# Kernel tuning notes

Measured on AMD Instinct MI355X. Metric: run time of the kernel, lower is better.

The kernel has to match this reference:

```python
import jax, jax.numpy as jnp
import numpy as np

N, E = 20000, 320000
IN, H, C = 1024, 8, 64
HC = H * C
EDGE_DIM = 16
NUM_GRAPHS = 8
LEAKY_SLOPE = 0.2
LN_EPS = 1e-5


def setup_inputs() -> dict:
    key = jax.random.key(0)
    ks = jax.random.split(key, 12)
    s = 0.05
    return {
        "x": jax.random.normal(ks[0], (N, IN), jnp.float32),
        "edge_attr": jax.random.normal(ks[1], (E, EDGE_DIM), jnp.float32),
        "edge_index": jax.random.randint(ks[2], (2, E), 0, N, dtype=jnp.int64),
        "batch": jnp.sort(jax.random.randint(ks[3], (N,), 0, NUM_GRAPHS, dtype=jnp.int64)),
        "W_src": jax.random.normal(ks[4], (IN, HC), jnp.float32) * s,
        "W_dst": jax.random.normal(ks[5], (IN, HC), jnp.float32) * s,
        "att_src": jax.random.normal(ks[6], (H, C), jnp.float32) * s,
        "att_dst": jax.random.normal(ks[7], (H, C), jnp.float32) * s,
        "bias": jnp.zeros((HC,), jnp.float32),
        "ln_gamma": jnp.ones((HC,), jnp.float32),
        "ln_beta": jnp.zeros((HC,), jnp.float32),
        "prelu_a": jnp.full((HC,), 0.25, jnp.float32),
    }


def reference(x, edge_attr, edge_index, batch, W_src, W_dst, att_src, att_dst,
              bias, ln_gamma, ln_beta, prelu_a):
    # Eval mode: node/edge feature dropout and attention dropout are identity.
    # with_edge == 'N': edge_attr is unused by the conv.
    n = x.shape[0]
    src, dst = edge_index[0], edge_index[1]

    xs = (x @ W_src).reshape(n, H, C)   # source-side projections
    xd = (x @ W_dst).reshape(n, H, C)   # dest-side projections
    a_src = jnp.einsum('nhc,hc->nh', xs, att_src)
    a_dst = jnp.einsum('nhc,hc->nh', xd, att_dst)

    # edge scores + softmax over incoming edges of each destination node
    e = jax.nn.leaky_relu(a_src[src] + a_dst[dst], LEAKY_SLOPE)  # [E,H]
    m = jax.ops.segment_max(e, dst, num_segments=n)              # [N,H]
    m = jax.lax.stop_gradient(jnp.where(jnp.isfinite(m), m, 0.0))
    ex = jnp.exp(e - m[dst])
    denom = jax.ops.segment_sum(ex, dst, num_segments=n)
    alpha = ex / (denom[dst] + 1e-16)                            # [E,H]

    msg = alpha[:, :, None] * xs[src]                            # [E,H,C]
    out = jax.ops.segment_sum(msg, dst, num_segments=n).reshape(n, HC) + bias

    # norm_type == 'layer': the per-graph boolean-mask loop applies LayerNorm
    # row-wise; with sorted batch ids this equals a single LayerNorm over all
    # nodes (LayerNorm has no cross-row statistics).
    mu = jnp.mean(out, axis=-1, keepdims=True)
    var = jnp.mean(jnp.square(out - mu), axis=-1, keepdims=True)
    y = (out - mu) * jax.lax.rsqrt(var + LN_EPS) * ln_gamma + ln_beta

    # PReLU with per-channel slope
    return jnp.where(y >= 0, y, prelu_a * y)
```

## Files before the change

kernel.cpp:

```cpp
#include <hip/hip_runtime.h>
#include <hip/hip_bf16.h>

#define N_NODES 20000
#define N_EDGES 320000
#define IN_DIM  1024
#define H_HEADS 8
#define C_CH    64
#define HC      512
#define LEAKY   0.2f
#define LN_EPS  1e-5f

#define BCOLS 576

typedef short bf16x8 __attribute__((ext_vector_type(8)));
typedef float f32x4  __attribute__((ext_vector_type(4)));

__device__ __forceinline__ unsigned short f2bf(float f) {
    union { float f; unsigned int u; } c; c.f = f;
    unsigned int u = c.u;
    unsigned int r = (u + 0x7fffu + ((u >> 16) & 1u)) >> 16;
    return (unsigned short)r;
}
__device__ __forceinline__ float bf2f(unsigned int h) {
    union { unsigned int u; float f; } c; c.u = h << 16; return c.f;
}
__device__ __forceinline__ void gload_lds16(const void* g, void* l) {
    __builtin_amdgcn_global_load_lds(
        (const __attribute__((address_space(1))) unsigned int*)g,
        (__attribute__((address_space(3))) unsigned int*)l, 16, 0, 0);
}

#define DEG_BLOCKS 1250

__global__ __launch_bounds__(256) void deg_hist(
        const int* __restrict__ ei, int* __restrict__ deg) {
    int e = blockIdx.x * 256 + threadIdx.x;
    atomicAdd(&deg[ei[N_EDGES + e]], 1);
}

#define CONV_BLOCKS 2048
#define PREP_BLOCKS 1024

__global__ __launch_bounds__(256) void mid_pass(
        const float* __restrict__ x, short* __restrict__ xb,
        const float* __restrict__ Wsrc, const float* __restrict__ Wdst,
        const float* __restrict__ att_src, const float* __restrict__ att_dst,
        short* __restrict__ wbT,
        const int* __restrict__ deg, int* __restrict__ off,
        int* __restrict__ cursor) {
    int t   = threadIdx.x;
    int bid = blockIdx.x;

    if (bid < CONV_BLOCKS) {
        const int total = N_NODES * IN_DIM / 8;
        int stride = CONV_BLOCKS * 256;
        for (int i = bid * 256 + t; i < total; i += stride) {
            float4 a = ((const float4*)x)[(size_t)i * 2];
            float4 b = ((const float4*)x)[(size_t)i * 2 + 1];
            uint4 r;
            r.x = (unsigned int)f2bf(a.x) | ((unsigned int)f2bf(a.y) << 16);
            r.y = (unsigned int)f2bf(a.z) | ((unsigned int)f2bf(a.w) << 16);
            r.z = (unsigned int)f2bf(b.x) | ((unsigned int)f2bf(b.y) << 16);
            r.w = (unsigned int)f2bf(b.z) | ((unsigned int)f2bf(b.w) << 16);
            *(uint4*)(&xb[(size_t)i * 8]) = r;
        }
        return;
    }

    if (bid < CONV_BLOCKS + PREP_BLOCKS) {
        if (t >= 128) return;
        int k = bid - CONV_BLOCKS;
        float4 v = *(const float4*)(Wsrc + (size_t)k * HC + t * 4);
        wbT[(size_t)(t * 4 + 0) * IN_DIM + k] = (short)f2bf(v.x);
        wbT[(size_t)(t * 4 + 1) * IN_DIM + k] = (short)f2bf(v.y);
        wbT[(size_t)(t * 4 + 2) * IN_DIM + k] = (short)f2bf(v.z);
        wbT[(size_t)(t * 4 + 3) * IN_DIM + k] = (short)f2bf(v.w);
        if (t < 16) {
            int h = t & 7;
            const float* W   = (t < 8) ? Wsrc : Wdst;
            const float* att = (t < 8) ? att_src : att_dst;
            float s = 0.f;
            #pragma unroll
            for (int c = 0; c < C_CH; ++c)
                s += W[(size_t)k * HC + h * C_CH + c] * att[h * C_CH + c];
            wbT[(size_t)(512 + t) * IN_DIM + k] = (short)f2bf(s);
        } else if (t < 64) {
            wbT[(size_t)(512 + t) * IN_DIM + k] = 0;
        }
        return;
    }

    if (t >= 128) return;
    __shared__ int wtot[2];
    int lane = t & 63, w = t >> 6;
    const int4* deg4 = (const int4*)deg;
    int s = 0;
    if (t < 125) {
        #pragma unroll
        for (int j = 0; j < 40; ++j) {
            int4 u = deg4[t * 40 + j];
            s += u.x + u.y + u.z + u.w;
        }
    }
    int v = s;
    #pragma unroll
    for (int o = 1; o < 64; o <<= 1) {
        int u = __shfl_up(v, o);
        if (lane >= o) v += u;
    }
    if (lane == 63) wtot[w] = v;
    __syncthreads();
    int add = (w == 1) ? wtot[0] : 0;
    int run = add + v - s;
    if (t < 125) {
        int4* off4 = (int4*)off;
        int4* cur4 = (int4*)cursor;
        #pragma unroll
        for (int j = 0; j < 40; ++j) {
            int4 u = deg4[t * 40 + j];
            int4 o_;
            o_.x = run;
            o_.y = o_.x + u.x;
            o_.z = o_.y + u.y;
            o_.w = o_.z + u.z;
            off4[t * 40 + j] = o_;
            cur4[t * 40 + j] = o_;
            run = o_.w + u.w;
        }
        if (t == 124) off[N_NODES] = run;
    }
}

#define BM 64
#define BN 96
#define BK 64
#define NCOLT (BCOLS / BN)
#define NROWT ((N_NODES + BM - 1) / BM)
#define NWG (NCOLT * NROWT)
#define KSTEPS (IN_DIM / BK)
#define A_SLOTS (BM * BK / 8)
#define B_SLOTS (BN * BK / 8)

__global__ __launch_bounds__(256) void gemm_scatter(
        const short* __restrict__ xb,
        const short* __restrict__ wbT,
        short* __restrict__ xsb,
        float* __restrict__ a_srcv,
        float* __restrict__ a_dstv,
        const int* __restrict__ ei,
        int* __restrict__ cursor,
        int* __restrict__ csr_src) {
    __shared__ short As[A_SLOTS * 8];
    __shared__ short Bs[B_SLOTS * 8];

    int t = threadIdx.x;

    if (blockIdx.x >= NWG) {
        int e = (blockIdx.x - NWG) * 256 + t;
        int d = ei[N_EDGES + e];
        int idx = atomicAdd(&cursor[d], 1);
        csr_src[idx] = ei[e];
        return;
    }

    int orig = blockIdx.x;
    const int q = NWG >> 3, r = NWG & 7;
    int xcd  = orig & 7;
    int wgid = (xcd < r ? xcd * (q + 1) : r * (q + 1) + (xcd - r) * q) + (orig >> 3);
    int col0 = (wgid % NCOLT) * BN;
    int row0 = (wgid / NCOLT) * BM;

    int lane = t & 63;
    int w    = t >> 6;
    int lr   = lane & 15;
    int lg   = lane >> 4;
    int sw   = lr & 7;
    int wr   = (w >> 1) * 32;
    int wc   = (w & 1) * 48;

    const short* a_base[2];
    #pragma unroll
    for (int i = 0; i < 2; ++i) {
        int s  = t + 256 * i;
        int m  = s >> 3;
        int kc = (s & 7) ^ (m & 7);
        int gm = row0 + m;
        if (gm >= N_NODES) gm = N_NODES - 1;
        a_base[i] = xb + (size_t)gm * IN_DIM + kc * 8;
    }
    const short* b_base[3];
    #pragma unroll
    for (int i = 0; i < 3; ++i) {
        int s  = t + 256 * i;
        int c  = s >> 3;
        int kc = (s & 7) ^ (c & 7);
        b_base[i] = wbT + (size_t)(col0 + c) * IN_DIM + kc * 8;
    }

    f32x4 acc[2][3] = {};

    for (int step = 0; step < KSTEPS; ++step) {
        int k0 = step * BK;
        #pragma unroll
        for (int i = 0; i < 2; ++i)
            gload_lds16(a_base[i] + k0, &As[(t + 256 * i) * 8]);
        #pragma unroll
        for (int i = 0; i < 3; ++i)
            gload_lds16(b_base[i] + k0, &Bs[(t + 256 * i) * 8]);
        asm volatile("s_waitcnt vmcnt(0)" ::: "memory");
        __builtin_amdgcn_s_barrier();

        #pragma unroll
        for (int ks = 0; ks < 2; ++ks) {
            int kc  = ks * 4 + lg;
            int kca = kc ^ sw;
            bf16x8 af[2], bfr[3];
            #pragma unroll
            for (int mi = 0; mi < 2; ++mi)
                af[mi] = *(const bf16x8*)(&As[((wr + mi * 16 + lr) * 8 + kca) * 8]);
            #pragma unroll
            for (int ni = 0; ni < 3; ++ni)
                bfr[ni] = *(const bf16x8*)(&Bs[((wc + ni * 16 + lr) * 8 + kca) * 8]);
            __builtin_amdgcn_s_setprio(1);
            #pragma unroll
            for (int mi = 0; mi < 2; ++mi)
                #pragma unroll
                for (int ni = 0; ni < 3; ++ni)
                    acc[mi][ni] = __builtin_amdgcn_mfma_f32_16x16x32_bf16(
                        af[mi], bfr[ni], acc[mi][ni], 0, 0, 0);
            __builtin_amdgcn_s_setprio(0);
        }
        __builtin_amdgcn_s_barrier();
    }

    #pragma unroll
    for (int mi = 0; mi < 2; ++mi) {
        #pragma unroll
        for (int rr = 0; rr < 4; ++rr) {
            int row = row0 + wr + mi * 16 + lg * 4 + rr;
            if (row >= N_NODES) continue;
            #pragma unroll
            for (int ni = 0; ni < 3; ++ni) {
                int col = col0 + wc + ni * 16 + lr;
                float v = acc[mi][ni][rr];
                if (col < 512)      xsb[(size_t)row * HC + col] = (short)f2bf(v);
                else if (col < 520) a_srcv[(size_t)row * 8 + (col - 512)] = v;
                else if (col < 528) a_dstv[(size_t)row * 8 + (col - 520)] = v;
            }
        }
    }
}

__global__ __launch_bounds__(256) void aggregate_ln(
        const int* __restrict__ off,
        const int* __restrict__ csr_src,
        const float* __restrict__ a_srcv,
        const float* __restrict__ a_dstv,
        const short* __restrict__ xsb,
        const float* __restrict__ bias,
        const float* __restrict__ gamma,
        const float* __restrict__ beta,
        const float* __restrict__ prelu_a,
        float* __restrict__ out) {
    int lane = threadIdx.x & 63;
    int n    = blockIdx.x * 4 + (threadIdx.x >> 6);
    int ch0  = lane * 8;
    int h    = lane >> 3;

    int start = off[n], end = off[n + 1];
    float ad  = a_dstv[(size_t)n * 8 + h];

    float acc[8] = {};
    float wsum = 0.f;

#define EDGE_ACC(sv)                                                          \
    do {                                                                      \
        float sc_ = a_srcv[(size_t)(sv) * 8 + h] + ad;                        \
        uint4 u_  = *(const uint4*)(xsb + (size_t)(sv) * HC + ch0);           \
        sc_ = (sc_ >= 0.f) ? sc_ : LEAKY * sc_;                               \
        float w_ = __expf(sc_);                                               \
        acc[0] = fmaf(w_, bf2f(u_.x & 0xffffu), acc[0]);                      \
        acc[1] = fmaf(w_, bf2f(u_.x >> 16),     acc[1]);                      \
        acc[2] = fmaf(w_, bf2f(u_.y & 0xffffu), acc[2]);                      \
        acc[3] = fmaf(w_, bf2f(u_.y >> 16),     acc[3]);                      \
        acc[4] = fmaf(w_, bf2f(u_.z & 0xffffu), acc[4]);                      \
        acc[5] = fmaf(w_, bf2f(u_.z >> 16),     acc[5]);                      \
        acc[6] = fmaf(w_, bf2f(u_.w & 0xffffu), acc[6]);                      \
        acc[7] = fmaf(w_, bf2f(u_.w >> 16),     acc[7]);                      \
        wsum += w_;                                                           \
    } while (0)

    int i = start;
    for (; i + 3 < end; i += 4) {
        int s0 = __builtin_amdgcn_readfirstlane(csr_src[i]);
        int s1 = __builtin_amdgcn_readfirstlane(csr_src[i + 1]);
        int s2 = __builtin_amdgcn_readfirstlane(csr_src[i + 2]);
        int s3 = __builtin_amdgcn_readfirstlane(csr_src[i + 3]);
        EDGE_ACC(s0); EDGE_ACC(s1); EDGE_ACC(s2); EDGE_ACC(s3);
    }
    for (; i < end; ++i) {
        int s0 = __builtin_amdgcn_readfirstlane(csr_src[i]);
        EDGE_ACC(s0);
    }
#undef EDGE_ACC

    float inv = 1.f / (wsum + 1e-16f);
    float4 b0 = *(const float4*)(bias + ch0);
    float4 b1 = *(const float4*)(bias + ch0 + 4);
    float v8[8];
    float psum = 0.f, psq = 0.f;
    const float bb[8] = {b0.x, b0.y, b0.z, b0.w, b1.x, b1.y, b1.z, b1.w};
    #pragma unroll
    for (int j = 0; j < 8; ++j) {
        v8[j] = acc[j] * inv + bb[j];
        psum += v8[j];
        psq  += v8[j] * v8[j];
    }
    #pragma unroll
    for (int o = 32; o > 0; o >>= 1) {
        psum += __shfl_xor(psum, o);
        psq  += __shfl_xor(psq, o);
    }
    float mu   = psum * (1.f / (float)HC);
    float var  = psq * (1.f / (float)HC) - mu * mu;
    float rstd = rsqrtf(var + LN_EPS);

    float4 g0 = *(const float4*)(gamma + ch0);
    float4 g1 = *(const float4*)(gamma + ch0 + 4);
    float4 e0 = *(const float4*)(beta + ch0);
    float4 e1 = *(const float4*)(beta + ch0 + 4);
    float4 p0 = *(const float4*)(prelu_a + ch0);
    float4 p1 = *(const float4*)(prelu_a + ch0 + 4);
    const float gg[8] = {g0.x, g0.y, g0.z, g0.w, g1.x, g1.y, g1.z, g1.w};
    const float ee[8] = {e0.x, e0.y, e0.z, e0.w, e1.x, e1.y, e1.z, e1.w};
    const float pp[8] = {p0.x, p0.y, p0.z, p0.w, p1.x, p1.y, p1.z, p1.w};
    float y[8];
    #pragma unroll
    for (int j = 0; j < 8; ++j) {
        float v = (v8[j] - mu) * rstd * gg[j] + ee[j];
        y[j] = (v >= 0.f) ? v : pp[j] * v;
    }
    float4* o4 = (float4*)(out + (size_t)n * HC + ch0);
    o4[0] = make_float4(y[0], y[1], y[2], y[3]);
    o4[1] = make_float4(y[4], y[5], y[6], y[7]);
}

extern "C" void kernel_launch(void* const* d_in, const int* in_sizes, int n_in,
                              void* d_out, int out_size, void* d_ws, size_t ws_size,
                              hipStream_t stream) {
    const float* x        = (const float*)d_in[0];
    const int*   ei       = (const int*)d_in[2];
    const float* Wsrc     = (const float*)d_in[4];
    const float* Wdst     = (const float*)d_in[5];
    const float* att_src  = (const float*)d_in[6];
    const float* att_dst  = (const float*)d_in[7];
    const float* bias     = (const float*)d_in[8];
    const float* gamma    = (const float*)d_in[9];
    const float* beta     = (const float*)d_in[10];
    const float* prelu_a  = (const float*)d_in[11];
    float* out            = (float*)d_out;

    char*  ws = (char*)d_ws;
    size_t o  = 0;
    auto alloc = [&](size_t bytes) -> void* {
        void* p = ws + o;
        o += (bytes + 255) & ~(size_t)255;
        return p;
    };
    short* wbT     = (short*)alloc(sizeof(short) * BCOLS * IN_DIM);
    short* xsb     = (short*)alloc(sizeof(short) * (size_t)N_NODES * HC);
    float* a_srcv  = (float*)alloc(sizeof(float) * N_NODES * 8);
    float* a_dstv  = (float*)alloc(sizeof(float) * N_NODES * 8);
    int*   deg     = (int*)alloc(sizeof(int) * N_NODES);
    int*   off     = (int*)alloc(sizeof(int) * (N_NODES + 1));
    int*   cursor  = (int*)alloc(sizeof(int) * N_NODES);
    int*   csr_src = (int*)alloc(sizeof(int) * N_EDGES);

    short* xb = (short*)d_out;

    hipMemsetAsync(deg, 0, sizeof(int) * N_NODES, stream);

    deg_hist<<<DEG_BLOCKS, 256, 0, stream>>>(ei, deg);

    mid_pass<<<CONV_BLOCKS + PREP_BLOCKS + 1, 256, 0, stream>>>(
        x, xb, Wsrc, Wdst, att_src, att_dst, wbT, deg, off, cursor);

    gemm_scatter<<<NWG + DEG_BLOCKS, 256, 0, stream>>>(
        xb, wbT, xsb, a_srcv, a_dstv, ei, cursor, csr_src);

    aggregate_ln<<<N_NODES / 4, 256, 0, stream>>>(
        off, csr_src, a_srcv, a_dstv, xsb, bias, gamma, beta, prelu_a, out);
}
```

Before: 152.9 us.

## Fuse fp32-to-bf16 conversion of x into GEMM A-tile load, widen N tile

```diff
diff --git a/kernel.cpp b/kernel.cpp
--- a/kernel.cpp
+++ b/kernel.cpp
@@ -24,6 +24,11 @@
 __device__ __forceinline__ float bf2f(unsigned int h) {
     union { unsigned int u; float f; } c; c.u = h << 16; return c.f;
 }
+__device__ __forceinline__ unsigned int cvtpk(float lo, float hi) {
+    unsigned int r;
+    asm("v_cvt_pk_bf16_f32 %0, %1, %2" : "=v"(r) : "v"(lo), "v"(hi));
+    return r;
+}
 __device__ __forceinline__ void gload_lds16(const void* g, void* l) {
     __builtin_amdgcn_global_load_lds(
         (const __attribute__((address_space(1))) unsigned int*)g,
@@ -38,101 +43,80 @@
     atomicAdd(&deg[ei[N_EDGES + e]], 1);
 }
 
-#define CONV_BLOCKS 2048
-#define PREP_BLOCKS 1024
-
-__global__ __launch_bounds__(256) void mid_pass(
-        const float* __restrict__ x, short* __restrict__ xb,
-        const float* __restrict__ Wsrc, const float* __restrict__ Wdst,
-        const float* __restrict__ att_src, const float* __restrict__ att_dst,
-        short* __restrict__ wbT,
-        const int* __restrict__ deg, int* __restrict__ off,
-        int* __restrict__ cursor) {
-    int t   = threadIdx.x;
-    int bid = blockIdx.x;
-
-    if (bid < CONV_BLOCKS) {
-        const int total = N_NODES * IN_DIM / 8;
-        int stride = CONV_BLOCKS * 256;
-        for (int i = bid * 256 + t; i < total; i += stride) {
-            float4 a = ((const float4*)x)[(size_t)i * 2];
-            float4 b = ((const float4*)x)[(size_t)i * 2 + 1];
-            uint4 r;
-            r.x = (unsigned int)f2bf(a.x) | ((unsigned int)f2bf(a.y) << 16);
-            r.y = (unsigned int)f2bf(a.z) | ((unsigned int)f2bf(a.w) << 16);
-            r.z = (unsigned int)f2bf(b.x) | ((unsigned int)f2bf(b.y) << 16);
-            r.w = (unsigned int)f2bf(b.z) | ((unsigned int)f2bf(b.w) << 16);
-            *(uint4*)(&xb[(size_t)i * 8]) = r;
+__global__ void prep_w_scan(const float* __restrict__ Wsrc,
+                            const float* __restrict__ Wdst,
+                            const float* __restrict__ att_src,
+                            const float* __restrict__ att_dst,
+                            short* __restrict__ wbT,
+                            const int* __restrict__ deg,
+                            int* __restrict__ off,
+                            int* __restrict__ cursor) {
+    int t = threadIdx.x;
+
+    if (blockIdx.x == IN_DIM) {
+        __shared__ int wtot[2];
+        int lane = t & 63, w = t >> 6;
+        const int4* deg4 = (const int4*)deg;
+        int s = 0;
+        if (t < 125) {
+            #pragma unroll
+            for (int j = 0; j < 40; ++j) {
+                int4 u = deg4[t * 40 + j];
+                s += u.x + u.y + u.z + u.w;
+            }
+        }
+        int v = s;
+        #pragma unroll
+        for (int o = 1; o < 64; o <<= 1) {
+            int u = __shfl_up(v, o);
+            if (lane >= o) v += u;
+        }
+        if (lane == 63) wtot[w] = v;
+        __syncthreads();
+        int add = (w == 1) ? wtot[0] : 0;
+        int run = add + v - s;
+        if (t < 125) {
+            int4* off4 = (int4*)off;
+            int4* cur4 = (int4*)cursor;
+            #pragma unroll
+            for (int j = 0; j < 40; ++j) {
+                int4 u = deg4[t * 40 + j];
+                int4 o_;
+                o_.x = run;
+                o_.y = o_.x + u.x;
+                o_.z = o_.y + u.y;
+                o_.w = o_.z + u.z;
+                off4[t * 40 + j] = o_;
+                cur4[t * 40 + j] = o_;
+                run = o_.w + u.w;
+            }
+            if (t == 124) off[N_NODES] = run;
         }
         return;
     }
 
-    if (bid < CONV_BLOCKS + PREP_BLOCKS) {
-        if (t >= 128) return;
-        int k = bid - CONV_BLOCKS;
-        float4 v = *(const float4*)(Wsrc + (size_t)k * HC + t * 4);
-        wbT[(size_t)(t * 4 + 0) * IN_DIM + k] = (short)f2bf(v.x);
-        wbT[(size_t)(t * 4 + 1) * IN_DIM + k] = (short)f2bf(v.y);
-        wbT[(size_t)(t * 4 + 2) * IN_DIM + k] = (short)f2bf(v.z);
-        wbT[(size_t)(t * 4 + 3) * IN_DIM + k] = (short)f2bf(v.w);
-        if (t < 16) {
-            int h = t & 7;
-            const float* W   = (t < 8) ? Wsrc : Wdst;
-            const float* att = (t < 8) ? att_src : att_dst;
-            float s = 0.f;
-            #pragma unroll
-            for (int c = 0; c < C_CH; ++c)
-                s += W[(size_t)k * HC + h * C_CH + c] * att[h * C_CH + c];
-            wbT[(size_t)(512 + t) * IN_DIM + k] = (short)f2bf(s);
-        } else if (t < 64) {
-            wbT[(size_t)(512 + t) * IN_DIM + k] = 0;
-        }
-        return;
-    }
-
-    if (t >= 128) return;
-    __shared__ int wtot[2];
-    int lane = t & 63, w = t >> 6;
-    const int4* deg4 = (const int4*)deg;
-    int s = 0;
-    if (t < 125) {
+    int k = blockIdx.x;
+    float4 v = *(const float4*)(Wsrc + (size_t)k * HC + t * 4);
+    wbT[(size_t)(t * 4 + 0) * IN_DIM + k] = (short)f2bf(v.x);
+    wbT[(size_t)(t * 4 + 1) * IN_DIM + k] = (short)f2bf(v.y);
+    wbT[(size_t)(t * 4 + 2) * IN_DIM + k] = (short)f2bf(v.z);
+    wbT[(size_t)(t * 4 + 3) * IN_DIM + k] = (short)f2bf(v.w);
+    if (t < 16) {
+        int h = t & 7;
+        const float* W   = (t < 8) ? Wsrc : Wdst;
+        const float* att = (t < 8) ? att_src : att_dst;
+        float s = 0.f;
         #pragma unroll
-        for (int j = 0; j < 40; ++j) {
-            int4 u = deg4[t * 40 + j];
-            s += u.x + u.y + u.z + u.w;
-        }
-    }
-    int v = s;
-    #pragma unroll
-    for (int o = 1; o < 64; o <<= 1) {
-        int u = __shfl_up(v, o);
-        if (lane >= o) v += u;
-    }
-    if (lane == 63) wtot[w] = v;
-    __syncthreads();
-    int add = (w == 1) ? wtot[0] : 0;
-    int run = add + v - s;
-    if (t < 125) {
-        int4* off4 = (int4*)off;
-        int4* cur4 = (int4*)cursor;
-        #pragma unroll
-        for (int j = 0; j < 40; ++j) {
-            int4 u = deg4[t * 40 + j];
-            int4 o_;
-            o_.x = run;
-            o_.y = o_.x + u.x;
-            o_.z = o_.y + u.y;
-            o_.w = o_.z + u.z;
-            off4[t * 40 + j] = o_;
-            cur4[t * 40 + j] = o_;
-            run = o_.w + u.w;
-        }
-        if (t == 124) off[N_NODES] = run;
+        for (int c = 0; c < C_CH; ++c)
+            s += W[(size_t)k * HC + h * C_CH + c] * att[h * C_CH + c];
+        wbT[(size_t)(512 + t) * IN_DIM + k] = (short)f2bf(s);
+    } else if (t < 64) {
+        wbT[(size_t)(512 + t) * IN_DIM + k] = 0;
     }
 }
 
 #define BM 64
-#define BN 96
+#define BN 192
 #define BK 64
 #define NCOLT (BCOLS / BN)
 #define NROWT ((N_NODES + BM - 1) / BM)
@@ -142,7 +126,7 @@
 #define B_SLOTS (BN * BK / 8)
 
 __global__ __launch_bounds__(256) void gemm_scatter(
-        const short* __restrict__ xb,
+        const float* __restrict__ x,
         const short* __restrict__ wbT,
         short* __restrict__ xsb,
         float* __restrict__ a_srcv,
@@ -176,9 +160,9 @@
     int lg   = lane >> 4;
     int sw   = lr & 7;
     int wr   = (w >> 1) * 32;
-    int wc   = (w & 1) * 48;
-
-    const short* a_base[2];
+    int wc   = (w & 1) * 96;
+
+    const float* a_base[2];
     #pragma unroll
     for (int i = 0; i < 2; ++i) {
         int s  = t + 256 * i;
@@ -186,51 +170,60 @@
         int kc = (s & 7) ^ (m & 7);
         int gm = row0 + m;
         if (gm >= N_NODES) gm = N_NODES - 1;
-        a_base[i] = xb + (size_t)gm * IN_DIM + kc * 8;
-    }
-    const short* b_base[3];
-    #pragma unroll
-    for (int i = 0; i < 3; ++i) {
+        a_base[i] = x + (size_t)gm * IN_DIM + kc * 8;
+    }
+    const short* b_base[6];
+    #pragma unroll
+    for (int i = 0; i < 6; ++i) {
         int s  = t + 256 * i;
         int c  = s >> 3;
         int kc = (s & 7) ^ (c & 7);
         b_base[i] = wbT + (size_t)(col0 + c) * IN_DIM + kc * 8;
     }
 
-    f32x4 acc[2][3] = {};
+    f32x4 acc[2][6] = {};
 
     for (int step = 0; step < KSTEPS; ++step) {
         int k0 = step * BK;
-        #pragma unroll
-        for (int i = 0; i < 2; ++i)
-            gload_lds16(a_base[i] + k0, &As[(t + 256 * i) * 8]);
-        #pragma unroll
-        for (int i = 0; i < 3; ++i)
-            gload_lds16(b_base[i] + k0, &Bs[(t + 256 * i) * 8]);
-        asm volatile("s_waitcnt vmcnt(0)" ::: "memory");
-        __builtin_amdgcn_s_barrier();
+        {
+            float4 fa0 = *(const float4*)(a_base[0] + k0);
+            float4 fb0 = *(const float4*)(a_base[0] + k0 + 4);
+            float4 fa1 = *(const float4*)(a_base[1] + k0);
+            float4 fb1 = *(const float4*)(a_base[1] + k0 + 4);
+            #pragma unroll
+            for (int i = 0; i < 6; ++i)
+                gload_lds16(b_base[i] + k0, &Bs[(t + 256 * i) * 8]);
+            uint4 r0, r1;
+            r0.x = cvtpk(fa0.x, fa0.y);  r0.y = cvtpk(fa0.z, fa0.w);
+            r0.z = cvtpk(fb0.x, fb0.y);  r0.w = cvtpk(fb0.z, fb0.w);
+            r1.x = cvtpk(fa1.x, fa1.y);  r1.y = cvtpk(fa1.z, fa1.w);
+            r1.z = cvtpk(fb1.x, fb1.y);  r1.w = cvtpk(fb1.z, fb1.w);
+            *(uint4*)(&As[(t      ) * 8]) = r0;
+            *(uint4*)(&As[(t + 256) * 8]) = r1;
+        }
+        __syncthreads();
 
         #pragma unroll
         for (int ks = 0; ks < 2; ++ks) {
             int kc  = ks * 4 + lg;
             int kca = kc ^ sw;
-            bf16x8 af[2], bfr[3];
+            bf16x8 af[2], bfr[6];
             #pragma unroll
             for (int mi = 0; mi < 2; ++mi)
                 af[mi] = *(const bf16x8*)(&As[((wr + mi * 16 + lr) * 8 + kca) * 8]);
             #pragma unroll
-            for (int ni = 0; ni < 3; ++ni)
+            for (int ni = 0; ni < 6; ++ni)
                 bfr[ni] = *(const bf16x8*)(&Bs[((wc + ni * 16 + lr) * 8 + kca) * 8]);
             __builtin_amdgcn_s_setprio(1);
             #pragma unroll
             for (int mi = 0; mi < 2; ++mi)
                 #pragma unroll
-                for (int ni = 0; ni < 3; ++ni)
+                for (int ni = 0; ni < 6; ++ni)
                     acc[mi][ni] = __builtin_amdgcn_mfma_f32_16x16x32_bf16(
                         af[mi], bfr[ni], acc[mi][ni], 0, 0, 0);
             __builtin_amdgcn_s_setprio(0);
         }
-        __builtin_amdgcn_s_barrier();
+        __syncthreads();
     }
 
     #pragma unroll
@@ -240,7 +233,7 @@
             int row = row0 + wr + mi * 16 + lg * 4 + rr;
             if (row >= N_NODES) continue;
             #pragma unroll
-            for (int ni = 0; ni < 3; ++ni) {
+            for (int ni = 0; ni < 6; ++ni) {
                 int col = col0 + wc + ni * 16 + lr;
                 float v = acc[mi][ni][rr];
                 if (col < 512)      xsb[(size_t)row * HC + col] = (short)f2bf(v);
@@ -376,17 +369,15 @@
     int*   cursor  = (int*)alloc(sizeof(int) * N_NODES);
     int*   csr_src = (int*)alloc(sizeof(int) * N_EDGES);
 
-    short* xb = (short*)d_out;
-
     hipMemsetAsync(deg, 0, sizeof(int) * N_NODES, stream);
 
     deg_hist<<<DEG_BLOCKS, 256, 0, stream>>>(ei, deg);
 
-    mid_pass<<<CONV_BLOCKS + PREP_BLOCKS + 1, 256, 0, stream>>>(
-        x, xb, Wsrc, Wdst, att_src, att_dst, wbT, deg, off, cursor);
+    prep_w_scan<<<IN_DIM + 1, 128, 0, stream>>>(Wsrc, Wdst, att_src, att_dst,
+                                                wbT, deg, off, cursor);
 
     gemm_scatter<<<NWG + DEG_BLOCKS, 256, 0, stream>>>(
-        xb, wbT, xsb, a_srcv, a_dstv, ei, cursor, csr_src);
+        x, wbT, xsb, a_srcv, a_dstv, ei, cursor, csr_src);
 
     aggregate_ln<<<N_NODES / 4, 256, 0, stream>>>(
         off, csr_src, a_srcv, a_dstv, xsb, bias, gamma, beta, prelu_a, out);
```

Result: no change. 152.2 us (-0.5%).
